# Optimization experiments

Hardware: AMD Instinct MI355X
Metric: run time of the kernel (lower is better)

## Reference

```python
import jax, jax.numpy as jnp
import numpy as np

N, E, F, H, O, G = 100000, 1600000, 128, 128, 64, 1024


def _prelu(x, a):
    return jnp.where(x >= 0, x, a * x)


def _gcn_conv(h, src, dst, w, W, b, n_nodes):
    # GCNConv with scalar edge weights and weight-1 self loops.
    deg = jax.ops.segment_sum(w, dst, num_segments=n_nodes) + 1.0  # [N]
    dis = jax.lax.rsqrt(deg)                                       # deg^-1/2
    hW = h @ W.T                                                   # [N,H]
    coef = (w * dis[src] * dis[dst])[:, None]                      # [E,1]
    agg = jax.ops.segment_sum(hW[src] * coef, dst, num_segments=n_nodes)
    agg = agg + hW * (1.0 / deg)[:, None]                          # self loops
    return agg + b


def setup_inputs() -> dict:
    key = jax.random.key(0)
    ks = jax.random.split(key, 12)
    x = jax.random.normal(ks[0], (N, F), dtype=jnp.float32)
    edge_index = jax.random.randint(ks[1], (2, E), 0, N, dtype=jnp.int64)
    edge_attr = jax.random.uniform(ks[2], (E,), dtype=jnp.float32)
    batch = jnp.sort(jax.random.randint(ks[3], (N,), 0, G, dtype=jnp.int64))
    s = lambda fan_in: 1.0 / np.sqrt(fan_in)
    fc1_w = jax.random.uniform(ks[4], (H, F), jnp.float32, -s(F), s(F))
    fc1_b = jax.random.uniform(ks[5], (H,), jnp.float32, -s(F), s(F))
    gc1_w = jax.random.uniform(ks[6], (H, H), jnp.float32, -s(H), s(H))
    gc1_b = jnp.zeros((H,), jnp.float32)
    gc2_w = jax.random.uniform(ks[7], (H, H), jnp.float32, -s(H), s(H))
    gc2_b = jnp.zeros((H,), jnp.float32)
    fc2_w = jax.random.uniform(ks[8], (O, H), jnp.float32, -s(H), s(H))
    fc2_b = jax.random.uniform(ks[9], (O,), jnp.float32, -s(H), s(H))
    a_fc1 = jnp.float32(0.25)
    a_gc1 = jnp.float32(0.25)
    a_gc2 = jnp.float32(0.25)
    return dict(x=x, edge_index=edge_index, edge_attr=edge_attr, batch=batch,
                fc1_w=fc1_w, fc1_b=fc1_b, gc1_w=gc1_w, gc1_b=gc1_b,
                gc2_w=gc2_w, gc2_b=gc2_b, fc2_w=fc2_w, fc2_b=fc2_b,
                a_fc1=a_fc1, a_gc1=a_gc1, a_gc2=a_gc2)


def reference(x, edge_index, edge_attr, batch, fc1_w, fc1_b, gc1_w, gc1_b,
              gc2_w, gc2_b, fc2_w, fc2_b, a_fc1, a_gc1, a_gc2):
    n_nodes = x.shape[0]
    src, dst = edge_index[0], edge_index[1]
    h = _prelu(x @ fc1_w.T + fc1_b, a_fc1)
    h = _prelu(_gcn_conv(h, src, dst, edge_attr, gc1_w, gc1_b, n_nodes), a_gc1)
    h = _prelu(_gcn_conv(h, src, dst, edge_attr, gc2_w, gc2_b, n_nodes), a_gc2)
    # global mean pool over graphs
    sums = jax.ops.segment_sum(h, batch, num_segments=G)
    cnt = jax.ops.segment_sum(jnp.ones((n_nodes,), h.dtype), batch, num_segments=G)
    hg = sums / jnp.maximum(cnt, 1.0)[:, None]
    # L2 normalize (torch normalize, eps=1e-12)
    hg = hg / jnp.maximum(jnp.linalg.norm(hg, axis=1, keepdims=True), 1e-12)
    return hg @ fc2_w.T + fc2_b
```

## Files before the change

kernel.cpp:

```cpp
#include <hip/hip_runtime.h>
#include <hip/hip_fp16.h>


#define CHK 1024
typedef unsigned int u32;
using f16 = _Float16;
using f16x8 = __attribute__((ext_vector_type(8))) _Float16;
using f32x4 = __attribute__((ext_vector_type(4))) float;

__global__ __launch_bounds__(256) void k_hist(const int* __restrict__ dst,
                                              const float* __restrict__ w,
                                              int* __restrict__ cnt,
                                              float* __restrict__ degf, int E) {
  int e = blockIdx.x * 256 + threadIdx.x;
  if (e < E) {
    int d = dst[e];
    atomicAdd(&cnt[d], 1);
    atomicAdd(&degf[d], w[e]);
  }
}

__global__ __launch_bounds__(256) void k_dis(const float* __restrict__ degf,
                                             float* __restrict__ dis,
                                             float* __restrict__ inv, int N) {
  int n = blockIdx.x * 256 + threadIdx.x;
  if (n < N) {
    float deg = degf[n] + 1.0f;
    dis[n] = rsqrtf(deg);
    inv[n] = 1.0f / deg;
  }
}

__global__ __launch_bounds__(256) void k_scan_reduce(const int* __restrict__ cnt,
                                                     int* __restrict__ chunkSum, int N) {
  __shared__ int sd[256];
  int b = blockIdx.x, t = threadIdx.x;
  int base = b * CHK + t * 4;
  int s = 0;
#pragma unroll
  for (int i = 0; i < 4; i++)
    if (base + i < N) s += cnt[base + i];
  sd[t] = s;
  __syncthreads();
  for (int off = 128; off; off >>= 1) {
    if (t < off) sd[t] += sd[t + off];
    __syncthreads();
  }
  if (t == 0) chunkSum[b] = sd[0];
}

__global__ void k_scan_chunks(const int* __restrict__ chunkSum,
                              int* __restrict__ chunkOff, int NC) {
  if (threadIdx.x == 0 && blockIdx.x == 0) {
    int s = 0;
    for (int i = 0; i < NC; i++) {
      chunkOff[i] = s;
      s += chunkSum[i];
    }
  }
}

__global__ __launch_bounds__(256) void k_scan_final(const int* __restrict__ cnt,
                                                    const int* __restrict__ chunkOff,
                                                    int* __restrict__ rowptr,
                                                    int* __restrict__ cursor, int N, int E) {
  __shared__ int sd[256];
  int b = blockIdx.x, t = threadIdx.x;
  int base = b * CHK + t * 4;
  int v[4], loc[4];
#pragma unroll
  for (int i = 0; i < 4; i++) v[i] = (base + i < N) ? cnt[base + i] : 0;
  loc[0] = 0;
  loc[1] = v[0];
  loc[2] = v[0] + v[1];
  loc[3] = v[0] + v[1] + v[2];
  int tot = loc[3] + v[3];
  sd[t] = tot;
  __syncthreads();
  for (int off = 1; off < 256; off <<= 1) {
    int xv = (t >= off) ? sd[t - off] : 0;
    __syncthreads();
    sd[t] += xv;
    __syncthreads();
  }
  int tbase = (t ? sd[t - 1] : 0) + chunkOff[b];
#pragma unroll
  for (int i = 0; i < 4; i++) {
    if (base + i < N) {
      int r = tbase + loc[i];
      rowptr[base + i] = r;
      cursor[base + i] = r;
    }
  }
  if (b == 0 && t == 0) rowptr[N] = E;
}

__global__ __launch_bounds__(256) void k_scatter(const int* __restrict__ src,
                                                 const int* __restrict__ dst,
                                                 const float* __restrict__ w,
                                                 const float* __restrict__ dis,
                                                 int* __restrict__ cursor,
                                                 int2* __restrict__ csr, int E) {
  int e = blockIdx.x * 256 + threadIdx.x;
  if (e < E) {
    int s = src[e], d = dst[e];
    float c = w[e] * dis[s] * dis[d];
    int p = atomicAdd(&cursor[d], 1);
    int2 v;
    v.x = s;
    v.y = __float_as_int(c);
    csr[p] = v;
  }
}

__global__ __launch_bounds__(256) void k_prep_bfrag(const float* __restrict__ W,
                                                    f16x8* __restrict__ Bf) {
  int t = blockIdx.x * 256 + threadIdx.x;
  int combo = t >> 6;
  int l = t & 63;
  int o = (combo & 7) * 16 + (l & 15);
  int k0 = (combo >> 3) * 32 + (l >> 4) * 8;
  f16x8 b;
#pragma unroll
  for (int i = 0; i < 8; i++) b[i] = (f16)W[o * 128 + k0 + i];
  Bf[combo * 64 + l] = b;
}

template <bool FP32_IN, bool BIAS>
__global__ __launch_bounds__(256) void k_gemm_mfma(const f16* __restrict__ Ah,
                                                   const float* __restrict__ Af,
                                                   const f16x8* __restrict__ Bf,
                                                   f16* __restrict__ out,
                                                   const float* __restrict__ bias,
                                                   const float* __restrict__ slope,
                                                   int N) {
  __shared__ f16 ls[64 * 128];
  int t = threadIdx.x;
  int w = t >> 6, l = t & 63;
  int l15 = l & 15, kgrp = l >> 4;
  int nodeBase = blockIdx.x * 64 + w * 16;
  f32x4 acc[8];
#pragma unroll
  for (int ct = 0; ct < 8; ct++)
#pragma unroll
    for (int j = 0; j < 4; j++) acc[ct][j] = 0.f;

  int arow = nodeBase + l15;
  if (arow >= N) arow = N - 1;
#pragma unroll
  for (int kc = 0; kc < 4; kc++) {
    f16x8 a;
    if (FP32_IN) {
      const float4* p0 = (const float4*)(Af + (size_t)arow * 128 + kc * 32 + kgrp * 8);
      float4 x0 = p0[0], x1 = p0[1];
      a[0] = (f16)x0.x; a[1] = (f16)x0.y; a[2] = (f16)x0.z; a[3] = (f16)x0.w;
      a[4] = (f16)x1.x; a[5] = (f16)x1.y; a[6] = (f16)x1.z; a[7] = (f16)x1.w;
    } else {
      a = *(const f16x8*)(Ah + (size_t)arow * 128 + kc * 32 + kgrp * 8);
    }
#pragma unroll
    for (int ct = 0; ct < 8; ct++) {
      f16x8 b = Bf[(kc * 8 + ct) * 64 + l];
      acc[ct] = __builtin_amdgcn_mfma_f32_16x16x32_f16(a, b, acc[ct], 0, 0, 0);
    }
  }
  float sl = BIAS ? *slope : 0.f;
  f16* slab = ls + w * 16 * 128;
#pragma unroll
  for (int ct = 0; ct < 8; ct++) {
    float bv = BIAS ? bias[ct * 16 + l15] : 0.f;
#pragma unroll
    for (int j = 0; j < 4; j++) {
      float v = acc[ct][j];
      if (BIAS) {
        v += bv;
        v = v >= 0.f ? v : sl * v;
      }
      slab[(kgrp * 4 + j) * 128 + ct * 16 + l15] = (f16)v;
    }
  }
  __syncthreads();
  {
    int r = l >> 2;
    int gnode = nodeBase + r;
    if (gnode < N) {
      const uint4* srcp = (const uint4*)(slab + r * 128);
      uint4* dstp = (uint4*)(out + (size_t)gnode * 128);
#pragma unroll
      for (int i = 0; i < 4; i++) {
        int chunk = (l & 3) + i * 4;
        dstp[chunk] = srcp[chunk];
      }
    }
  }
}

template <bool POOL>
__global__ __launch_bounds__(256) void k_agg_h(const __half2* __restrict__ hW,
                                               const int* __restrict__ rowptr,
                                               const int2* __restrict__ csr,
                                               const float* __restrict__ inv,
                                               const float* __restrict__ bias,
                                               const float* __restrict__ slope,
                                               const int* __restrict__ batch,
                                               __half2* __restrict__ outh,
                                               float* __restrict__ pool,
                                               float* __restrict__ cntg, int N) {
  int wid = (blockIdx.x * 256 + threadIdx.x) >> 6;
  if (wid >= N) return;
  int l = threadIdx.x & 63;
  int r0 = rowptr[wid], r1 = rowptr[wid + 1];
  float2 acc;
  {
    float2 f = __half22float2(hW[(size_t)wid * 64 + l]);
    float iv = inv[wid];
    acc.x = f.x * iv;
    acc.y = f.y * iv;
  }
  for (int base = r0; base < r1; base += 64) {
    int idx = base + l;
    int sl = 0;
    float cl = 0.f;
    if (idx < r1) {
      int2 e = csr[idx];
      sl = e.x;
      cl = __int_as_float(e.y);
    }
    int m = min(64, r1 - base);
    for (int k = 0; k < m; k += 8) {
      __half2 v[8];
      float c[8];
#pragma unroll
      for (int i = 0; i < 8; i++) {
        int s = __shfl(sl, k + i);
        c[i] = __shfl(cl, k + i);
        v[i] = hW[(size_t)s * 64 + l];
      }
#pragma unroll
      for (int i = 0; i < 8; i++) {
        float2 f = __half22float2(v[i]);
        acc.x += f.x * c[i];
        acc.y += f.y * c[i];
      }
    }
  }
  float a = *slope;
  float2 b = *(const float2*)&bias[l * 2];
  acc.x += b.x;
  acc.y += b.y;
  acc.x = acc.x >= 0.f ? acc.x : a * acc.x;
  acc.y = acc.y >= 0.f ? acc.y : a * acc.y;
  if (POOL) {
    int g = batch[wid];
    atomicAdd(&pool[(size_t)g * 128 + l * 2], acc.x);
    atomicAdd(&pool[(size_t)g * 128 + l * 2 + 1], acc.y);
    if (l == 0) atomicAdd(&cntg[g], 1.0f);
  } else {
    outh[(size_t)wid * 64 + l] = __float22half2_rn(acc);
  }
}

__global__ __launch_bounds__(64) void k_final(const float* __restrict__ pool,
                                              const float* __restrict__ cntg,
                                              const float* __restrict__ fc2w,
                                              const float* __restrict__ fc2b,
                                              float* __restrict__ out) {
  __shared__ float hg[128];
  int g = blockIdx.x, l = threadIdx.x;
  float cnt = cntg[g];
  float ic = 1.0f / fmaxf(cnt, 1.0f);
  float2 v = *(const float2*)&pool[(size_t)g * 128 + l * 2];
  v.x *= ic;
  v.y *= ic;
  float ss = v.x * v.x + v.y * v.y;
#pragma unroll
  for (int off = 1; off < 64; off <<= 1) ss += __shfl_xor(ss, off);
  float nrm = sqrtf(ss);
  float sc = 1.0f / fmaxf(nrm, 1e-12f);
  hg[l * 2] = v.x * sc;
  hg[l * 2 + 1] = v.y * sc;
  __syncthreads();
  float acc = fc2b[l];
#pragma unroll 4
  for (int k = 0; k < 128; k++) acc += hg[k] * fc2w[l * 128 + k];
  out[(size_t)g * 64 + l] = acc;
}

extern "C" void kernel_launch(void* const* d_in, const int* in_sizes, int n_in,
                              void* d_out, int out_size, void* d_ws, size_t ws_size,
                              hipStream_t stream) {
  const float* x = (const float*)d_in[0];
  const int* ei = (const int*)d_in[1];
  const float* ew = (const float*)d_in[2];
  const int* batch = (const int*)d_in[3];
  const float* fc1_w = (const float*)d_in[4];
  const float* fc1_b = (const float*)d_in[5];
  const float* gc1_w = (const float*)d_in[6];
  const float* gc1_b = (const float*)d_in[7];
  const float* gc2_w = (const float*)d_in[8];
  const float* gc2_b = (const float*)d_in[9];
  const float* fc2_w = (const float*)d_in[10];
  const float* fc2_b = (const float*)d_in[11];
  const float* a_fc1 = (const float*)d_in[12];
  const float* a_gc1 = (const float*)d_in[13];
  const float* a_gc2 = (const float*)d_in[14];

  int N = in_sizes[0] / 128;
  int E = in_sizes[2];
  int G = out_size / 64;
  const int* src = ei;
  const int* dst = ei + E;

  char* p = (char*)d_ws;
  auto carve = [&](size_t bytes) -> char* {
    char* r = p;
    p += (bytes + 255) & ~(size_t)255;
    return r;
  };
  f16* bufA = (f16*)carve((size_t)N * 128 * 2);
  f16* bufH = (f16*)carve((size_t)N * 128 * 2);
  int2* csr = (int2*)carve((size_t)E * 8);
  int* cnt = (int*)carve((size_t)N * 4);
  int* rowptr = (int*)carve((size_t)(N + 1) * 4);
  int* cursor = (int*)carve((size_t)N * 4);
  float* degf = (float*)carve((size_t)N * 4);
  float* dis = (float*)carve((size_t)N * 4);
  float* inv = (float*)carve((size_t)N * 4);
  f16x8* Bf1 = (f16x8*)carve(2048 * 16);
  f16x8* Bf2 = (f16x8*)carve(2048 * 16);
  f16x8* Bf3 = (f16x8*)carve(2048 * 16);
  int NC = (N + CHK - 1) / CHK;
  int* chunkSum = (int*)carve((size_t)NC * 4);
  int* chunkOff = (int*)carve((size_t)NC * 4);
  float* pool = (float*)carve((size_t)G * 128 * 4);
  float* cntg = (float*)carve((size_t)G * 4);

  hipMemsetAsync(cnt, 0, (size_t)N * 4, stream);
  hipMemsetAsync(degf, 0, (size_t)N * 4, stream);
  hipMemsetAsync(pool, 0, (size_t)G * 128 * 4, stream);
  hipMemsetAsync(cntg, 0, (size_t)G * 4, stream);

  k_prep_bfrag<<<8, 256, 0, stream>>>(fc1_w, Bf1);
  k_prep_bfrag<<<8, 256, 0, stream>>>(gc1_w, Bf2);
  k_prep_bfrag<<<8, 256, 0, stream>>>(gc2_w, Bf3);

  int gE = (E + 255) / 256;
  int gN = (N + 255) / 256;
  k_hist<<<gE, 256, 0, stream>>>(dst, ew, cnt, degf, E);
  k_dis<<<gN, 256, 0, stream>>>(degf, dis, inv, N);
  k_scan_reduce<<<NC, 256, 0, stream>>>(cnt, chunkSum, N);
  k_scan_chunks<<<1, 64, 0, stream>>>(chunkSum, chunkOff, NC);
  k_scan_final<<<NC, 256, 0, stream>>>(cnt, chunkOff, rowptr, cursor, N, E);
  k_scatter<<<gE, 256, 0, stream>>>(src, dst, ew, dis, cursor, csr, E);

  int gGemm = (N + 63) / 64;
  k_gemm_mfma<true, true><<<gGemm, 256, 0, stream>>>(nullptr, x, Bf1, bufA, fc1_b, a_fc1, N);
  k_gemm_mfma<false, false><<<gGemm, 256, 0, stream>>>(bufA, nullptr, Bf2, bufH, nullptr, nullptr, N);
  int gAgg = (int)(((size_t)N * 64 + 255) / 256);
  k_agg_h<false><<<gAgg, 256, 0, stream>>>((const __half2*)bufH, rowptr, csr, inv, gc1_b,
                                           a_gc1, batch, (__half2*)bufA, nullptr, cntg, N);
  k_gemm_mfma<false, false><<<gGemm, 256, 0, stream>>>(bufA, nullptr, Bf3, bufH, nullptr, nullptr, N);
  k_agg_h<true><<<gAgg, 256, 0, stream>>>((const __half2*)bufH, rowptr, csr, inv, gc2_b,
                                          a_gc2, batch, nullptr, pool, cntg, N);
  k_final<<<G, 64, 0, stream>>>(pool, cntg, fc2_w, fc2_b, (float*)d_out);
}
```

Before: 567.4 us.

## Replace pull-based CSR aggregation with push-based CSC scatter using fp16 packed atomics

The graph is now bucketed by source node instead of destination. Each wave reads its own feature row once and scatters scaled copies to its neighbours with global_atomic_pk_add_f16. The GEMM writes the self-loop term into an fp16 accumulator, and a separate elementwise epilogue applies bias, PReLU and pooling. This removes random gathers of neighbour rows but adds 1.6M×64 contended fp16 atomics. Accumulating in fp16 also loses precision compared with fp32 register accumulation.

```diff
diff --git a/kernel.cpp b/kernel.cpp
--- a/kernel.cpp
+++ b/kernel.cpp
@@ -8,15 +8,20 @@
 using f16x8 = __attribute__((ext_vector_type(8))) _Float16;
 using f32x4 = __attribute__((ext_vector_type(4))) float;
 
-__global__ __launch_bounds__(256) void k_hist(const int* __restrict__ dst,
+__device__ inline void atomic_pk_add_h2(__half2* addr, __half2 val) {
+  asm volatile("global_atomic_pk_add_f16 %0, %1, off"
+               :: "v"(addr), "v"(val) : "memory");
+}
+
+__global__ __launch_bounds__(256) void k_hist(const int* __restrict__ src,
+                                              const int* __restrict__ dst,
                                               const float* __restrict__ w,
                                               int* __restrict__ cnt,
                                               float* __restrict__ degf, int E) {
   int e = blockIdx.x * 256 + threadIdx.x;
   if (e < E) {
-    int d = dst[e];
-    atomicAdd(&cnt[d], 1);
-    atomicAdd(&degf[d], w[e]);
+    atomicAdd(&cnt[src[e]], 1);
+    atomicAdd(&degf[dst[e]], w[e]);
   }
 }
 
@@ -100,16 +105,16 @@
                                                  const float* __restrict__ w,
                                                  const float* __restrict__ dis,
                                                  int* __restrict__ cursor,
-                                                 int2* __restrict__ csr, int E) {
+                                                 int2* __restrict__ csc, int E) {
   int e = blockIdx.x * 256 + threadIdx.x;
   if (e < E) {
     int s = src[e], d = dst[e];
     float c = w[e] * dis[s] * dis[d];
-    int p = atomicAdd(&cursor[d], 1);
+    int p = atomicAdd(&cursor[s], 1);
     int2 v;
-    v.x = s;
+    v.x = d;
     v.y = __float_as_int(c);
-    csr[p] = v;
+    csc[p] = v;
   }
 }
 
@@ -126,11 +131,13 @@
   Bf[combo * 64 + l] = b;
 }
 
-template <bool FP32_IN, bool BIAS>
+template <bool FP32_IN, bool BIAS, bool SELF>
 __global__ __launch_bounds__(256) void k_gemm_mfma(const f16* __restrict__ Ah,
                                                    const float* __restrict__ Af,
                                                    const f16x8* __restrict__ Bf,
                                                    f16* __restrict__ out,
+                                                   __half2* __restrict__ accum,
+                                                   const float* __restrict__ inv,
                                                    const float* __restrict__ bias,
                                                    const float* __restrict__ slope,
                                                    int N) {
@@ -186,77 +193,85 @@
     if (gnode < N) {
       const uint4* srcp = (const uint4*)(slab + r * 128);
       uint4* dstp = (uint4*)(out + (size_t)gnode * 128);
+      __half2 iv2;
+      uint4* dsto = nullptr;
+      if (SELF) {
+        iv2 = __float2half2_rn(inv[gnode]);
+        dsto = (uint4*)(accum + (size_t)gnode * 64);
+      }
 #pragma unroll
       for (int i = 0; i < 4; i++) {
         int chunk = (l & 3) + i * 4;
-        dstp[chunk] = srcp[chunk];
+        uint4 q = srcp[chunk];
+        dstp[chunk] = q;
+        if (SELF) {
+          __half2* qh = (__half2*)&q;
+#pragma unroll
+          for (int j = 0; j < 4; j++) qh[j] = __hmul2(qh[j], iv2);
+          dsto[chunk] = q;
+        }
       }
     }
   }
 }
 
-template <bool POOL>
-__global__ __launch_bounds__(256) void k_agg_h(const __half2* __restrict__ hW,
-                                               const int* __restrict__ rowptr,
-                                               const int2* __restrict__ csr,
-                                               const float* __restrict__ inv,
-                                               const float* __restrict__ bias,
-                                               const float* __restrict__ slope,
-                                               const int* __restrict__ batch,
-                                               __half2* __restrict__ outh,
-                                               float* __restrict__ pool,
-                                               float* __restrict__ cntg, int N) {
+__global__ __launch_bounds__(256) void k_push(const __half2* __restrict__ hW,
+                                              const int* __restrict__ rowptr,
+                                              const int2* __restrict__ csc,
+                                              __half2* __restrict__ accum, int N) {
   int wid = (blockIdx.x * 256 + threadIdx.x) >> 6;
   if (wid >= N) return;
   int l = threadIdx.x & 63;
   int r0 = rowptr[wid], r1 = rowptr[wid + 1];
-  float2 acc;
-  {
-    float2 f = __half22float2(hW[(size_t)wid * 64 + l]);
-    float iv = inv[wid];
-    acc.x = f.x * iv;
-    acc.y = f.y * iv;
-  }
-  for (int base = r0; base < r1; base += 64) {
-    int idx = base + l;
-    int sl = 0;
-    float cl = 0.f;
-    if (idx < r1) {
-      int2 e = csr[idx];
-      sl = e.x;
-      cl = __int_as_float(e.y);
-    }
-    int m = min(64, r1 - base);
-    for (int k = 0; k < m; k += 8) {
-      __half2 v[8];
-      float c[8];
-#pragma unroll
-      for (int i = 0; i < 8; i++) {
-        int s = __shfl(sl, k + i);
-        c[i] = __shfl(cl, k + i);
-        v[i] = hW[(size_t)s * 64 + l];
-      }
-#pragma unroll
-      for (int i = 0; i < 8; i++) {
-        float2 f = __half22float2(v[i]);
-        acc.x += f.x * c[i];
-        acc.y += f.y * c[i];
-      }
-    }
-  }
+  r0 = __builtin_amdgcn_readfirstlane(r0);
+  r1 = __builtin_amdgcn_readfirstlane(r1);
+  if (r0 == r1) return;
+  __half2 row = hW[(u32)wid * 64u + (u32)l];
+  int e = r0;
+  for (; e + 4 <= r1; e += 4) {
+    int2 e0 = csc[e], e1 = csc[e + 1], e2 = csc[e + 2], e3 = csc[e + 3];
+    __half2 s0 = __hmul2(row, __float2half2_rn(__int_as_float(e0.y)));
+    __half2 s1 = __hmul2(row, __float2half2_rn(__int_as_float(e1.y)));
+    __half2 s2 = __hmul2(row, __float2half2_rn(__int_as_float(e2.y)));
+    __half2 s3 = __hmul2(row, __float2half2_rn(__int_as_float(e3.y)));
+    atomic_pk_add_h2(&accum[(u32)e0.x * 64u + (u32)l], s0);
+    atomic_pk_add_h2(&accum[(u32)e1.x * 64u + (u32)l], s1);
+    atomic_pk_add_h2(&accum[(u32)e2.x * 64u + (u32)l], s2);
+    atomic_pk_add_h2(&accum[(u32)e3.x * 64u + (u32)l], s3);
+  }
+  for (; e < r1; ++e) {
+    int2 en = csc[e];
+    __half2 s = __hmul2(row, __float2half2_rn(__int_as_float(en.y)));
+    atomic_pk_add_h2(&accum[(u32)en.x * 64u + (u32)l], s);
+  }
+}
+
+template <bool POOL>
+__global__ __launch_bounds__(256) void k_epi(const __half2* __restrict__ acc,
+                                             const float* __restrict__ bias,
+                                             const float* __restrict__ slope,
+                                             const int* __restrict__ batch,
+                                             __half2* __restrict__ outh,
+                                             float* __restrict__ pool,
+                                             float* __restrict__ cntg, int N) {
+  int i = blockIdx.x * 256 + threadIdx.x;
+  if (i >= N * 64) return;
+  int l = i & 63;
+  float2 v = __half22float2(acc[i]);
   float a = *slope;
   float2 b = *(const float2*)&bias[l * 2];
-  acc.x += b.x;
-  acc.y += b.y;
-  acc.x = acc.x >= 0.f ? acc.x : a * acc.x;
-  acc.y = acc.y >= 0.f ? acc.y : a * acc.y;
+  v.x += b.x;
+  v.y += b.y;
+  v.x = v.x >= 0.f ? v.x : a * v.x;
+  v.y = v.y >= 0.f ? v.y : a * v.y;
   if (POOL) {
-    int g = batch[wid];
-    atomicAdd(&pool[(size_t)g * 128 + l * 2], acc.x);
-    atomicAdd(&pool[(size_t)g * 128 + l * 2 + 1], acc.y);
+    int n = i >> 6;
+    int g = batch[n];
+    atomicAdd(&pool[(size_t)g * 128 + l * 2], v.x);
+    atomicAdd(&pool[(size_t)g * 128 + l * 2 + 1], v.y);
     if (l == 0) atomicAdd(&cntg[g], 1.0f);
   } else {
-    outh[(size_t)wid * 64 + l] = __float22half2_rn(acc);
+    outh[i] = __float22half2_rn(v);
   }
 }
 
@@ -319,7 +334,8 @@
   };
   f16* bufA = (f16*)carve((size_t)N * 128 * 2);
   f16* bufH = (f16*)carve((size_t)N * 128 * 2);
-  int2* csr = (int2*)carve((size_t)E * 8);
+  __half2* bufO = (__half2*)carve((size_t)N * 64 * 4);
+  int2* csc = (int2*)carve((size_t)E * 8);
   int* cnt = (int*)carve((size_t)N * 4);
   int* rowptr = (int*)carve((size_t)(N + 1) * 4);
   int* cursor = (int*)carve((size_t)N * 4);
@@ -346,21 +362,31 @@
 
   int gE = (E + 255) / 256;
   int gN = (N + 255) / 256;
-  k_hist<<<gE, 256, 0, stream>>>(dst, ew, cnt, degf, E);
+  k_hist<<<gE, 256, 0, stream>>>(src, dst, ew, cnt, degf, E);
   k_dis<<<gN, 256, 0, stream>>>(degf, dis, inv, N);
   k_scan_reduce<<<NC, 256, 0, stream>>>(cnt, chunkSum, N);
   k_scan_chunks<<<1, 64, 0, stream>>>(chunkSum, chunkOff, NC);
   k_scan_final<<<NC, 256, 0, stream>>>(cnt, chunkOff, rowptr, cursor, N, E);
-  k_scatter<<<gE, 256, 0, stream>>>(src, dst, ew, dis, cursor, csr, E);
+  k_scatter<<<gE, 256, 0, stream>>>(src, dst, ew, dis, cursor, csc, E);
 
   int gGemm = (N + 63) / 64;
-  k_gemm_mfma<true, true><<<gGemm, 256, 0, stream>>>(nullptr, x, Bf1, bufA, fc1_b, a_fc1, N);
-  k_gemm_mfma<false, false><<<gGemm, 256, 0, stream>>>(bufA, nullptr, Bf2, bufH, nullptr, nullptr, N);
-  int gAgg = (int)(((size_t)N * 64 + 255) / 256);
-  k_agg_h<false><<<gAgg, 256, 0, stream>>>((const __half2*)bufH, rowptr, csr, inv, gc1_b,
-                                           a_gc1, batch, (__half2*)bufA, nullptr, cntg, N);
-  k_gemm_mfma<false, false><<<gGemm, 256, 0, stream>>>(bufA, nullptr, Bf3, bufH, nullptr, nullptr, N);
-  k_agg_h<true><<<gAgg, 256, 0, stream>>>((const __half2*)bufH, rowptr, csr, inv, gc2_b,
-                                          a_gc2, batch, nullptr, pool, cntg, N);
+  int gWave = (int)(((size_t)N * 64 + 255) / 256);
+  int gElem = gWave;
+
+  k_gemm_mfma<true, true, false><<<gGemm, 256, 0, stream>>>(
+      nullptr, x, Bf1, bufA, nullptr, nullptr, fc1_b, a_fc1, N);
+
+  k_gemm_mfma<false, false, true><<<gGemm, 256, 0, stream>>>(
+      bufA, nullptr, Bf2, bufH, bufO, inv, nullptr, nullptr, N);
+  k_push<<<gWave, 256, 0, stream>>>((const __half2*)bufH, rowptr, csc, bufO, N);
+  k_epi<false><<<gElem, 256, 0, stream>>>(bufO, gc1_b, a_gc1, batch,
+                                          (__half2*)bufA, nullptr, cntg, N);
+
+  k_gemm_mfma<false, false, true><<<gGemm, 256, 0, stream>>>(
+      bufA, nullptr, Bf3, bufH, bufO, inv, nullptr, nullptr, N);
+  k_push<<<gWave, 256, 0, stream>>>((const __half2*)bufH, rowptr, csc, bufO, N);
+  k_epi<true><<<gElem, 256, 0, stream>>>(bufO, gc2_b, a_gc2, batch,
+                                         nullptr, pool, cntg, N);
+
   k_final<<<G, 64, 0, stream>>>(pool, cntg, fc2_w, fc2_b, (float*)d_out);
 }
```

New measurement: 1.137 ms. 2x slower.

## Gather four edges per wave with 16-byte loads in GCN aggregation

Applied to the files above, without the earlier changes.

The aggregation kernel now splits each 64-lane wave into four 16-lane groups. Each group gathers a different neighbor's fp16 feature row with 16-byte vector loads, instead of one edge per wave-wide 4-byte load. Partial sums are combined across groups with xor shuffles, and only 16 lanes apply the self-loop, bias, PReLU and the store or pool atomics. This aims to raise memory-level parallelism and cut per-edge instruction overhead, but it adds cross-lane reduction cost and leaves most lanes idle in the epilogue.

```diff
diff --git a/kernel.cpp b/kernel.cpp
--- a/kernel.cpp
+++ b/kernel.cpp
@@ -196,27 +196,25 @@
 }
 
 template <bool POOL>
-__global__ __launch_bounds__(256) void k_agg_h(const __half2* __restrict__ hW,
+__global__ __launch_bounds__(256) void k_agg_v(const f16* __restrict__ hW,
                                                const int* __restrict__ rowptr,
                                                const int2* __restrict__ csr,
                                                const float* __restrict__ inv,
                                                const float* __restrict__ bias,
                                                const float* __restrict__ slope,
                                                const int* __restrict__ batch,
-                                               __half2* __restrict__ outh,
+                                               f16* __restrict__ outh,
                                                float* __restrict__ pool,
                                                float* __restrict__ cntg, int N) {
   int wid = (blockIdx.x * 256 + threadIdx.x) >> 6;
   if (wid >= N) return;
   int l = threadIdx.x & 63;
+  int g = l >> 4, sub = l & 15;
   int r0 = rowptr[wid], r1 = rowptr[wid + 1];
-  float2 acc;
-  {
-    float2 f = __half22float2(hW[(size_t)wid * 64 + l]);
-    float iv = inv[wid];
-    acc.x = f.x * iv;
-    acc.y = f.y * iv;
-  }
+  float acc[8];
+#pragma unroll
+  for (int j = 0; j < 8; j++) acc[j] = 0.f;
+
   for (int base = r0; base < r1; base += 64) {
     int idx = base + l;
     int sl = 0;
@@ -227,36 +225,70 @@
       cl = __int_as_float(e.y);
     }
     int m = min(64, r1 - base);
-    for (int k = 0; k < m; k += 8) {
-      __half2 v[8];
-      float c[8];
+    for (int k = 0; k < m; k += 32) {
+      int nin = min(32, m - k);
+      int ninstr = (nin + 3) >> 2;
+      uint4 v[8];
+      float cc[8];
 #pragma unroll
       for (int i = 0; i < 8; i++) {
-        int s = __shfl(sl, k + i);
-        c[i] = __shfl(cl, k + i);
-        v[i] = hW[(size_t)s * 64 + l];
+        if (i < ninstr) {
+          int ei = k + i * 4 + g;
+          int ec = ei < m ? ei : m - 1;
+          int s = __shfl(sl, ec);
+          float c = __shfl(cl, ec);
+          cc[i] = ei < m ? c : 0.f;
+          v[i] = *(const uint4*)(hW + (size_t)s * 128 + sub * 8);
+        }
       }
 #pragma unroll
       for (int i = 0; i < 8; i++) {
-        float2 f = __half22float2(v[i]);
-        acc.x += f.x * c[i];
-        acc.y += f.y * c[i];
+        if (i < ninstr) {
+          const __half2* hp = (const __half2*)&v[i];
+#pragma unroll
+          for (int j = 0; j < 4; j++) {
+            float2 f = __half22float2(hp[j]);
+            acc[2 * j] += f.x * cc[i];
+            acc[2 * j + 1] += f.y * cc[i];
+          }
+        }
       }
     }
   }
-  float a = *slope;
-  float2 b = *(const float2*)&bias[l * 2];
-  acc.x += b.x;
-  acc.y += b.y;
-  acc.x = acc.x >= 0.f ? acc.x : a * acc.x;
-  acc.y = acc.y >= 0.f ? acc.y : a * acc.y;
-  if (POOL) {
-    int g = batch[wid];
-    atomicAdd(&pool[(size_t)g * 128 + l * 2], acc.x);
-    atomicAdd(&pool[(size_t)g * 128 + l * 2 + 1], acc.y);
-    if (l == 0) atomicAdd(&cntg[g], 1.0f);
-  } else {
-    outh[(size_t)wid * 64 + l] = __float22half2_rn(acc);
+#pragma unroll
+  for (int off = 16; off < 64; off <<= 1)
+#pragma unroll
+    for (int j = 0; j < 8; j++) acc[j] += __shfl_xor(acc[j], off);
+
+  if (l < 16) {
+    uint4 ov = *(const uint4*)(hW + (size_t)wid * 128 + sub * 8);
+    const __half2* op = (const __half2*)&ov;
+    float iv = inv[wid];
+    float a = *slope;
+    float res[8];
+#pragma unroll
+    for (int j = 0; j < 4; j++) {
+      float2 f = __half22float2(op[j]);
+      float2 b = *(const float2*)&bias[sub * 8 + j * 2];
+      float vx = acc[2 * j] + f.x * iv + b.x;
+      float vy = acc[2 * j + 1] + f.y * iv + b.y;
+      res[2 * j] = vx >= 0.f ? vx : a * vx;
+      res[2 * j + 1] = vy >= 0.f ? vy : a * vy;
+    }
+    if (POOL) {
+      int gb = batch[wid];
+#pragma unroll
+      for (int j = 0; j < 8; j++)
+        atomicAdd(&pool[(size_t)gb * 128 + sub * 8 + j], res[j]);
+      if (sub == 0) atomicAdd(&cntg[gb], 1.0f);
+    } else {
+      uint4 q;
+      __half2* qh = (__half2*)&q;
+#pragma unroll
+      for (int j = 0; j < 4; j++)
+        qh[j] = __float22half2_rn(make_float2(res[2 * j], res[2 * j + 1]));
+      *(uint4*)(outh + (size_t)wid * 128 + sub * 8) = q;
+    }
   }
 }
 
@@ -354,13 +386,14 @@
   k_scatter<<<gE, 256, 0, stream>>>(src, dst, ew, dis, cursor, csr, E);
 
   int gGemm = (N + 63) / 64;
+  int gAgg = (int)(((size_t)N * 64 + 255) / 256);
+
   k_gemm_mfma<true, true><<<gGemm, 256, 0, stream>>>(nullptr, x, Bf1, bufA, fc1_b, a_fc1, N);
   k_gemm_mfma<false, false><<<gGemm, 256, 0, stream>>>(bufA, nullptr, Bf2, bufH, nullptr, nullptr, N);
-  int gAgg = (int)(((size_t)N * 64 + 255) / 256);
-  k_agg_h<false><<<gAgg, 256, 0, stream>>>((const __half2*)bufH, rowptr, csr, inv, gc1_b,
-                                           a_gc1, batch, (__half2*)bufA, nullptr, cntg, N);
+  k_agg_v<false><<<gAgg, 256, 0, stream>>>(bufH, rowptr, csr, inv, gc1_b, a_gc1, batch,
+                                           bufA, nullptr, cntg, N);
   k_gemm_mfma<false, false><<<gGemm, 256, 0, stream>>>(bufA, nullptr, Bf3, bufH, nullptr, nullptr, N);
-  k_agg_h<true><<<gAgg, 256, 0, stream>>>((const __half2*)bufH, rowptr, csr, inv, gc2_b,
-                                          a_gc2, batch, nullptr, pool, cntg, N);
+  k_agg_v<true><<<gAgg, 256, 0, stream>>>(bufH, rowptr, csr, inv, gc2_b, a_gc2, batch,
+                                          nullptr, pool, cntg, N);
   k_final<<<G, 64, 0, stream>>>(pool, cntg, fc2_w, fc2_b, (float*)d_out);
 }
```

Measured after the change: 904.9 us. 59.5% more time.
